# Kernel optimization log

Hardware: AMD Instinct MI355X
Metric: run time of the kernel (lower is better)

Reference implementation:

```python
import jax, jax.numpy as jnp
import numpy as np

NUM_HEADS = 8
NUM_NEIGHBORS = 32


def setup_inputs() -> dict:
    key = jax.random.key(0)
    ks = jax.random.split(key, 5)
    B, S, F, C = 4, 2048, 512, 3
    x = jax.random.normal(ks[0], (B, S, F), dtype=jnp.float32)
    coords = jax.random.uniform(ks[1], (B, S, C), dtype=jnp.float32)
    scale = 1.0 / np.sqrt(F)
    Wq = jax.random.normal(ks[2], (F, F), dtype=jnp.float32) * scale
    Wk = jax.random.normal(ks[3], (F, F), dtype=jnp.float32) * scale
    Wv = jax.random.normal(ks[4], (F, F), dtype=jnp.float32) * scale
    return {"x": x, "coords": coords, "Wq": Wq, "Wk": Wk, "Wv": Wv}


def _nearest_neighbors(coords, k):
    # coords: [B,S,C] -> dists [B,S,S]; drop self (index 0 after argsort)
    diff = coords[:, None, :, :] - coords[:, :, None, :]
    dists = jnp.linalg.norm(diff, axis=-1)
    return jnp.argsort(dists, axis=-1)[:, :, 1:k + 1]  # [B,S,K]


def reference(x, coords, Wq, Wk, Wv):
    B, S, F = x.shape
    H = NUM_HEADS
    D = F // H

    nn_idx = _nearest_neighbors(coords, NUM_NEIGHBORS)  # [B,S,K] int
    # dense boolean neighbor mask [B,S,S]: mask[b,q,kv] = kv in nn_idx[b,q]
    b_ix = jnp.arange(B)[:, None, None]
    q_ix = jnp.arange(S)[None, :, None]
    mask = jnp.zeros((B, S, S), dtype=bool).at[b_ix, q_ix, nn_idx].set(True)

    q = (x @ Wq.T).reshape(B, S, H, D).transpose(0, 2, 1, 3)  # [B,H,S,D]
    k = (x @ Wk.T).reshape(B, S, H, D).transpose(0, 2, 1, 3)
    v = (x @ Wv.T).reshape(B, S, H, D).transpose(0, 2, 1, 3)

    scale = 1.0 / jnp.sqrt(jnp.asarray(D, dtype=x.dtype))
    scores = jnp.einsum("bhqd,bhkd->bhqk", q, k) * scale
    neg_inf = jnp.asarray(-jnp.inf, dtype=scores.dtype)
    scores = jnp.where(mask[:, None, :, :], scores, neg_inf)
    attn = jax.nn.softmax(scores, axis=-1)
    out = jnp.einsum("bhqk,bhkd->bhqd", attn, v)  # [B,H,S,D]
    out = out.transpose(0, 2, 1, 3).reshape(B, S, F)
    metric = k.mean(axis=2)  # [B,H,D]
    return out, metric
```

## Files before the change

kernel.cpp:

```cpp
#include <hip/hip_runtime.h>
#include <stdint.h>

#define BATCH 4
#define SEQ   2048
#define FDIM  512
#define NHEAD 8
#define HDIM  64
#define KNN   32

typedef unsigned int u32;
typedef unsigned long long u64;
typedef unsigned short u16;
typedef unsigned short bf16_t;

typedef __attribute__((ext_vector_type(8))) short short8;
typedef __attribute__((ext_vector_type(4))) float f32x4;

#define SF  ((size_t)SEQ * FDIM)
#define BSF ((size_t)BATCH * SF)

#define CAST_NB 2432
#define XPART_NB 128

__device__ __forceinline__ bf16_t f2bf(float f) {
    u32 x = __float_as_uint(f);
    return (bf16_t)((x + 0x7FFFu + ((x >> 16) & 1u)) >> 16);
}
__device__ __forceinline__ float bf2f(bf16_t u) { return __uint_as_float(((u32)u) << 16); }
__device__ __forceinline__ void bf2x2(u32 p, float& a, float& b) {
    a = __uint_as_float(p << 16);
    b = __uint_as_float(p & 0xFFFF0000u);
}
__device__ __forceinline__ u64 min_u64(u64 a, u64 b) { return a < b ? a : b; }
__device__ __forceinline__ u64 shfl_xor_u64(u64 v, int m) {
    int lo = __shfl_xor((int)(u32)v, m, 64);
    int hi = __shfl_xor((int)(u32)(v >> 32), m, 64);
    return (((u64)(u32)hi) << 32) | (u32)lo;
}

__device__ __forceinline__ void gld16(const bf16_t* gp, bf16_t* lp) {
    __builtin_amdgcn_global_load_lds(
        (const __attribute__((address_space(1))) u32*)gp,
        (__attribute__((address_space(3))) u32*)lp, 16, 0, 0);
}

template <int CTRL>
__device__ __forceinline__ float dppf(float x) {
    return __int_as_float(__builtin_amdgcn_update_dpp(
        0, __float_as_int(x), CTRL, 0xF, 0xF, true));
}

__device__ __forceinline__ float dot8(uint4 k, f32x4 qa, f32x4 qb) {
    float f0, f1, f2, f3, f4, f5, f6, f7;
    bf2x2(k.x, f0, f1); bf2x2(k.y, f2, f3);
    bf2x2(k.z, f4, f5); bf2x2(k.w, f6, f7);
    return qa.x * f0 + qa.y * f1 + qa.z * f2 + qa.w * f3
         + qb.x * f4 + qb.y * f5 + qb.z * f6 + qb.w * f7;
}

__device__ __forceinline__ void acc8(uint4 v, float w, float* o) {
    float f0, f1, f2, f3, f4, f5, f6, f7;
    bf2x2(v.x, f0, f1); bf2x2(v.y, f2, f3);
    bf2x2(v.z, f4, f5); bf2x2(v.w, f6, f7);
    o[0] += w * f0; o[1] += w * f1; o[2] += w * f2; o[3] += w * f3;
    o[4] += w * f4; o[5] += w * f5; o[6] += w * f6; o[7] += w * f7;
}

__device__ __forceinline__ void cast_body(int cid,
                                          const float* __restrict__ x,
                                          const float* __restrict__ wq,
                                          const float* __restrict__ wk,
                                          const float* __restrict__ wv,
                                          bf16_t* __restrict__ xb,
                                          bf16_t* __restrict__ wqb,
                                          bf16_t* __restrict__ wkb,
                                          bf16_t* __restrict__ wvb) {
    int z, blk;
    if (cid < 2048) { z = 0; blk = cid; }
    else { int d = cid - 2048; z = 1 + (d >> 7); blk = d & 127; }
    const float* src = (z == 0) ? x : (z == 1) ? wq : (z == 2) ? wk : wv;
    bf16_t* dst      = (z == 0) ? xb : (z == 1) ? wqb : (z == 2) ? wkb : wvb;
    size_t idx = (size_t)blk * 256 + threadIdx.x;
    const float4 a = ((const float4*)src)[idx * 2 + 0];
    const float4 b = ((const float4*)src)[idx * 2 + 1];
    uint4 o;
    o.x = (u32)f2bf(a.x) | ((u32)f2bf(a.y) << 16);
    o.y = (u32)f2bf(a.z) | ((u32)f2bf(a.w) << 16);
    o.z = (u32)f2bf(b.x) | ((u32)f2bf(b.y) << 16);
    o.w = (u32)f2bf(b.z) | ((u32)f2bf(b.w) << 16);
    ((uint4*)dst)[idx] = o;
}

__device__ __forceinline__ void xpart_body(int id, const float* __restrict__ x,
                                           float* __restrict__ xpart) {
    const int b = id >> 5, chunk = id & 31;
    const int tid = threadIdx.x;
    const float* xp = x + (size_t)b * SF + (size_t)chunk * 64 * FDIM;
    float s0 = 0.f, s1 = 0.f;
    for (int r = 0; r < 64; ++r) {
        s0 += xp[(size_t)r * FDIM + tid];
        s1 += xp[(size_t)r * FDIM + tid + 256];
    }
    float* dst = xpart + (size_t)id * FDIM;
    dst[tid]       = s0 * (1.f / 2048.f);
    dst[tid + 256] = s1 * (1.f / 2048.f);
}

__device__ __forceinline__ void knn_body(char* smem, int blk,
                                         const float* __restrict__ coords,
                                         u16* __restrict__ nn_out) {
    u32* chist = (u32*)smem;
    u32* fhist = (u32*)(smem + 256);
    u64* bk    = (u64*)(smem + 1280);
    u64* wpart = (u64*)(smem + 1792);
    u32* sc    = (u32*)(smem + 1824);
    const int b   = blk >> 11;
    const int qi  = blk & (SEQ - 1);
    const int t   = threadIdx.x;
    const int wid = t >> 6, lane = t & 63;
    const size_t qb = (size_t)blk * KNN;

    fhist[t & 255] = 0;
    if (t < 64) chist[t] = 0;
    if (t == 0) { sc[2] = 0; sc[3] = 0; }

    const float* cb = coords + (size_t)b * SEQ * 3;
    const float qx = cb[qi * 3 + 0];
    const float qy = cb[qi * 3 + 1];
    const float qz = cb[qi * 3 + 2];

    float dist[8];
    int   ib[8];
    u64 tmin = ~0ull;
#pragma unroll
    for (int i = 0; i < 8; ++i) {
        int c = i * 256 + t;
        float dx = __fsub_rn(cb[c * 3 + 0], qx);
        float dy = __fsub_rn(cb[c * 3 + 1], qy);
        float dz = __fsub_rn(cb[c * 3 + 2], qz);
        float d2 = __fadd_rn(__fadd_rn(__fmul_rn(dx, dx), __fmul_rn(dy, dy)),
                             __fmul_rn(dz, dz));
        dist[i] = __fsqrt_rn(d2);
        ib[i] = (int)(dist[i] * 8192.0f);
        u64 key = (((u64)__float_as_uint(dist[i])) << 32) | (u32)c;
        tmin = min_u64(tmin, key);
    }
    tmin = min_u64(tmin, shfl_xor_u64(tmin, 1));
    tmin = min_u64(tmin, shfl_xor_u64(tmin, 2));
    tmin = min_u64(tmin, shfl_xor_u64(tmin, 4));
    tmin = min_u64(tmin, shfl_xor_u64(tmin, 8));
    tmin = min_u64(tmin, shfl_xor_u64(tmin, 16));
    tmin = min_u64(tmin, shfl_xor_u64(tmin, 32));
    if (lane == 0) wpart[wid] = tmin;
    __syncthreads();

#pragma unroll
    for (int i = 0; i < 8; ++i) atomicAdd(&chist[ib[i] >> 8], 1u);
    const u64 M = min_u64(min_u64(wpart[0], wpart[1]),
                          min_u64(wpart[2], wpart[3]));
    __syncthreads();

    if (t < 64) {
        u32 h = chist[t];
        u32 cum = h;
#pragma unroll
        for (int d = 1; d < 64; d <<= 1) {
            u32 v = (u32)__shfl_up((int)cum, d, 64);
            if (t >= d) cum += v;
        }
        u64 bal = __ballot(cum >= 33);
        int Bc = __ffsll((long long)bal) - 1;
        u32 excl = cum - h;
        u32 base = (u32)__shfl((int)excl, Bc, 64);
        if (t == 0) { sc[0] = (u32)Bc; sc[1] = base; }
    }
    __syncthreads();

    {
        const int Bc = (int)sc[0];
#pragma unroll
        for (int i = 0; i < 8; ++i)
            if ((ib[i] >> 8) == Bc) atomicAdd(&fhist[ib[i] & 255], 1u);
    }
    __syncthreads();

    if (t < 64) {
        const u32 Bc = sc[0], base = sc[1];
        u32 f0 = fhist[t * 4 + 0], f1 = fhist[t * 4 + 1];
        u32 f2 = fhist[t * 4 + 2], f3 = fhist[t * 4 + 3];
        u32 s = f0 + f1 + f2 + f3;
        u32 cum = s;
#pragma unroll
        for (int d = 1; d < 64; d <<= 1) {
            u32 v = (u32)__shfl_up((int)cum, d, 64);
            if (t >= d) cum += v;
        }
        u32 E = base + (cum - s);
        u32 c0 = E + f0, c1 = c0 + f1, c2 = c1 + f2, c3 = c2 + f3;
        u64 bal = __ballot(c3 >= 33);
        int L = __ffsll((long long)bal) - 1;
        if (t == L) {
            int j = (c0 >= 33) ? 0 : (c1 >= 33) ? 1 : (c2 >= 33) ? 2 : 3;
            sc[4] = (Bc << 8) | (u32)(t * 4 + j);
        }
    }
    __syncthreads();

    {
        const int ibt = (int)sc[4];
#pragma unroll
        for (int i = 0; i < 8; ++i) {
            int c = i * 256 + t;
            u64 key = (((u64)__float_as_uint(dist[i])) << 32) | (u32)c;
            if (ib[i] < ibt) {
                if (key != M) {
                    u32 pos = atomicAdd(&sc[2], 1u);
                    nn_out[qb + pos] = (u16)c;
                }
            } else if (ib[i] == ibt) {
                u32 bp = atomicAdd(&sc[3], 1u);
                if (bp < 64) bk[bp] = key;
            }
        }
    }
    __syncthreads();

    if (t < 64) {
        const u32 m = sc[2];
        const int n = (int)min(sc[3], 64u);
        const int need = 32 - (int)m;
        u64 k = (t < n) ? bk[t] : ~0ull;
        if (k == M) k = ~0ull;
#pragma unroll 1
        for (int r = 0; r < need; ++r) {
            u64 g = k;
            g = min_u64(g, shfl_xor_u64(g, 1));
            g = min_u64(g, shfl_xor_u64(g, 2));
            g = min_u64(g, shfl_xor_u64(g, 4));
            g = min_u64(g, shfl_xor_u64(g, 8));
            g = min_u64(g, shfl_xor_u64(g, 16));
            g = min_u64(g, shfl_xor_u64(g, 32));
            if (k == g) {
                nn_out[qb + m + r] = (u16)(g & 0x7FF);
                k = ~0ull;
            }
        }
    }
}

__global__ __launch_bounds__(256) void fused_ck(const float* __restrict__ x,
                                                const float* __restrict__ wq,
                                                const float* __restrict__ wk,
                                                const float* __restrict__ wv,
                                                bf16_t* __restrict__ xb,
                                                bf16_t* __restrict__ wqb,
                                                bf16_t* __restrict__ wkb,
                                                bf16_t* __restrict__ wvb,
                                                const float* __restrict__ coords,
                                                u16* __restrict__ nn_out,
                                                float* __restrict__ xpart) {
    __shared__ __align__(16) char smem[1856];
    const int bid = blockIdx.x;
    if (bid < CAST_NB) {
        cast_body(bid, x, wq, wk, wv, xb, wqb, wkb, wvb);
    } else if (bid < CAST_NB + XPART_NB) {
        xpart_body(bid - CAST_NB, x, xpart);
    } else {
        knn_body(smem, bid - CAST_NB - XPART_NB, coords, nn_out);
    }
}

__global__ __launch_bounds__(256) void gemm_mfma(const bf16_t* __restrict__ xb,
                                                 const bf16_t* __restrict__ wqb,
                                                 const bf16_t* __restrict__ wkb,
                                                 const bf16_t* __restrict__ wvb,
                                                 float* __restrict__ qout,
                                                 bf16_t* __restrict__ kvout,
                                                 const float* __restrict__ xpart,
                                                 const float* __restrict__ Wkf,
                                                 float* __restrict__ metric) {
    __shared__ __align__(16) bf16_t As[128 * 32];
    __shared__ __align__(16) bf16_t Bs[128 * 32];
    const int z = blockIdx.z;
    const int tid  = threadIdx.x;

    if (z == 3) {
        const int id = blockIdx.y * 4 + blockIdx.x;
        if (id >= 8) return;
        float* xbarL = (float*)As;
        const int b = id >> 1;
        float a0 = 0.f, a1 = 0.f;
#pragma unroll 4
        for (int c = 0; c < 32; ++c) {
            const float* xp = xpart + (size_t)((b << 5) | c) * FDIM;
            a0 += xp[tid];
            a1 += xp[tid + 256];
        }
        xbarL[tid] = a0; xbarL[tid + 256] = a1;
        __syncthreads();
        const int f = ((id & 1) << 8) | tid;
        const float* wr = Wkf + (size_t)f * FDIM;
        float acc = 0.f;
#pragma unroll 4
        for (int kk = 0; kk < FDIM; kk += 4) {
            float4 wv = *(const float4*)(wr + kk);
            acc += xbarL[kk + 0] * wv.x + xbarL[kk + 1] * wv.y
                 + xbarL[kk + 2] * wv.z + xbarL[kk + 3] * wv.w;
        }
        metric[(b << 9) | f] = acc;
        return;
    }

    const bf16_t* W = (z == 0) ? wqb : (z == 1) ? wkb : wvb;
    const int wid  = tid >> 6, lane = tid & 63;
    const int m16  = lane & 15, quad = lane >> 4;
    const int wm   = (wid & 1) * 64;
    const int wn   = (wid >> 1) * 64;
    const int m0   = blockIdx.y * 128;
    const int n0   = blockIdx.x * 128;

    const int sr = tid >> 2, sc = (tid & 3) * 8;
    const bf16_t* agp = xb + (size_t)(m0 + sr) * FDIM + sc;
    const bf16_t* bgp = W  + (size_t)(n0 + sr) * FDIM + sc;
    bf16_t* lAs = As + tid * 8;
    bf16_t* lBs = Bs + tid * 8;

    f32x4 acc[4][4];
#pragma unroll
    for (int i = 0; i < 4; ++i)
#pragma unroll
        for (int j = 0; j < 4; ++j) acc[i][j] = (f32x4){0.f, 0.f, 0.f, 0.f};

#pragma unroll 1
    for (int k0 = 0; k0 < FDIM; k0 += 32) {
        __syncthreads();
        gld16(agp + k0,                      lAs);
        gld16(agp + (size_t)64 * FDIM + k0,  lAs + 2048);
        gld16(bgp + k0,                      lBs);
        gld16(bgp + (size_t)64 * FDIM + k0,  lBs + 2048);
        __asm__ volatile("s_waitcnt vmcnt(0)" ::: "memory");
        __syncthreads();

        short8 af[4], bfr[4];
#pragma unroll
        for (int i = 0; i < 4; ++i)
            af[i] = *(const short8*)(As + (wm + i * 16 + m16) * 32 + quad * 8);
#pragma unroll
        for (int j = 0; j < 4; ++j)
            bfr[j] = *(const short8*)(Bs + (wn + j * 16 + m16) * 32 + quad * 8);
#pragma unroll
        for (int i = 0; i < 4; ++i)
#pragma unroll
            for (int j = 0; j < 4; ++j)
                acc[i][j] = __builtin_amdgcn_mfma_f32_16x16x32_bf16(af[i], bfr[j],
                                                                    acc[i][j], 0, 0, 0);
    }

    if (z == 0) {
#pragma unroll
        for (int i = 0; i < 4; ++i) {
            const int rowb = m0 + wm + i * 16 + quad * 4;
#pragma unroll
            for (int r = 0; r < 4; ++r) {
                float* orow = qout + (size_t)(rowb + r) * FDIM + n0 + wn + m16;
                orow[ 0] = acc[i][0][r]; orow[16] = acc[i][1][r];
                orow[32] = acc[i][2][r]; orow[48] = acc[i][3][r];
            }
        }
    } else {
        bf16_t* base = kvout + (size_t)(z - 1) * BSF;
#pragma unroll
        for (int i = 0; i < 4; ++i) {
            const int rowb = m0 + wm + i * 16 + quad * 4;
#pragma unroll
            for (int r = 0; r < 4; ++r) {
                bf16_t* orow = base + (size_t)(rowb + r) * FDIM + n0 + wn + m16;
                orow[ 0] = f2bf(acc[i][0][r]); orow[16] = f2bf(acc[i][1][r]);
                orow[32] = f2bf(acc[i][2][r]); orow[48] = f2bf(acc[i][3][r]);
            }
        }
    }
}

__global__ __launch_bounds__(256, 6) void attn_kernel(const bf16_t* __restrict__ kv,
                                                      const u16* __restrict__ nn,
                                                      float* __restrict__ out) {
    __shared__ float qsl[4][64];
    __shared__ float osl[4][8][64];
    const int i   = blockIdx.x;
    const int b   = (i & 7) >> 1;
    const int jb  = ((i >> 3) << 1) | (i & 1);
    const int tid = threadIdx.x;
    const int wid = tid >> 6, lane = tid & 63;
    const int gid = (jb << 2) | wid;
    const int qi  = gid >> 3, h = gid & 7;
    const int blk = (b << 11) | qi;

    int sreg = 0;
    if (lane < KNN) sreg = (int)nn[(size_t)blk * KNN + lane] & (SEQ - 1);
    qsl[wid][lane] = out[(size_t)blk * FDIM + h * HDIM + lane];

    const int g3 = lane >> 3, l8 = lane & 7;
    const int r0 = __shfl(sreg,      g3, 64);
    const int r1 = __shfl(sreg,  8 + g3, 64);
    const int r2 = __shfl(sreg, 16 + g3, 64);
    const int r3 = __shfl(sreg, 24 + g3, 64);

    const bf16_t* base = kv + ((size_t)(b << 11)) * FDIM + h * HDIM + l8 * 8;
    const uint4 k0 = *(const uint4*)(base + (size_t)r0 * FDIM);
    const uint4 k1 = *(const uint4*)(base + (size_t)r1 * FDIM);
    const uint4 k2 = *(const uint4*)(base + (size_t)r2 * FDIM);
    const uint4 k3 = *(const uint4*)(base + (size_t)r3 * FDIM);
    const uint4 v0 = *(const uint4*)(base + BSF + (size_t)r0 * FDIM);
    const uint4 v1 = *(const uint4*)(base + BSF + (size_t)r1 * FDIM);
    const uint4 v2 = *(const uint4*)(base + BSF + (size_t)r2 * FDIM);
    const uint4 v3 = *(const uint4*)(base + BSF + (size_t)r3 * FDIM);

    __asm__ volatile("s_waitcnt lgkmcnt(0)" ::: "memory");
    __builtin_amdgcn_wave_barrier();
    const f32x4 qa = *(const f32x4*)&qsl[wid][l8 * 8];
    const f32x4 qb = *(const f32x4*)&qsl[wid][l8 * 8 + 4];

    float s0 = dot8(k0, qa, qb);
    float s1 = dot8(k1, qa, qb);
    float s2 = dot8(k2, qa, qb);
    float s3 = dot8(k3, qa, qb);
    s0 += dppf<0xB1>(s0); s0 += dppf<0x4E>(s0); s0 += dppf<0x141>(s0);
    s1 += dppf<0xB1>(s1); s1 += dppf<0x4E>(s1); s1 += dppf<0x141>(s1);
    s2 += dppf<0xB1>(s2); s2 += dppf<0x4E>(s2); s2 += dppf<0x141>(s2);
    s3 += dppf<0xB1>(s3); s3 += dppf<0x4E>(s3); s3 += dppf<0x141>(s3);
    s0 *= 0.125f; s1 *= 0.125f; s2 *= 0.125f; s3 *= 0.125f;

    float ml = fmaxf(fmaxf(s0, s1), fmaxf(s2, s3));
    ml = fmaxf(ml, dppf<0x140>(ml));
    ml = fmaxf(ml, __shfl_xor(ml, 16, 64));
    ml = fmaxf(ml, __shfl_xor(ml, 32, 64));
    const float e0 = __expf(s0 - ml), e1 = __expf(s1 - ml);
    const float e2 = __expf(s2 - ml), e3 = __expf(s3 - ml);
    float sl = (e0 + e1) + (e2 + e3);
    sl += dppf<0x140>(sl);
    sl += __shfl_xor(sl, 16, 64);
    sl += __shfl_xor(sl, 32, 64);
    const float rs = 1.0f / sl;
    const float w0 = e0 * rs, w1 = e1 * rs, w2 = e2 * rs, w3 = e3 * rs;

    float o[8] = {0.f, 0.f, 0.f, 0.f, 0.f, 0.f, 0.f, 0.f};
    acc8(v0, w0, o);
    acc8(v1, w1, o);
    acc8(v2, w2, o);
    acc8(v3, w3, o);

    *(f32x4*)&osl[wid][g3][l8 * 8]     = (f32x4){o[0], o[1], o[2], o[3]};
    *(f32x4*)&osl[wid][g3][l8 * 8 + 4] = (f32x4){o[4], o[5], o[6], o[7]};
    __asm__ volatile("s_waitcnt lgkmcnt(0)" ::: "memory");
    __builtin_amdgcn_wave_barrier();
    float r = osl[wid][0][lane];
#pragma unroll
    for (int g = 1; g < 8; ++g) r += osl[wid][g][lane];
    out[(size_t)blk * FDIM + h * HDIM + lane] = r;
}

extern "C" void kernel_launch(void* const* d_in, const int* in_sizes, int n_in,
                              void* d_out, int out_size, void* d_ws, size_t ws_size,
                              hipStream_t stream) {
    const float* x      = (const float*)d_in[0];
    const float* coords = (const float*)d_in[1];
    const float* Wq     = (const float*)d_in[2];
    const float* Wk     = (const float*)d_in[3];
    const float* Wv     = (const float*)d_in[4];
    float* out    = (float*)d_out;
    float* metric = out + BSF;

    char* p = (char*)d_ws;
    bf16_t* xb    = (bf16_t*)p;                      p += BSF * sizeof(bf16_t);
    bf16_t* wqb   = (bf16_t*)p;                      p += (size_t)FDIM * FDIM * sizeof(bf16_t);
    bf16_t* wkb   = (bf16_t*)p;                      p += (size_t)FDIM * FDIM * sizeof(bf16_t);
    bf16_t* wvb   = (bf16_t*)p;                      p += (size_t)FDIM * FDIM * sizeof(bf16_t);
    bf16_t* kv    = (bf16_t*)p;                      p += 2 * BSF * sizeof(bf16_t);
    u16*    nn    = (u16*)p;                         p += (size_t)BATCH * SEQ * KNN * sizeof(u16);
    float*  xpart = (float*)p;

    fused_ck<<<CAST_NB + XPART_NB + BATCH * SEQ, 256, 0, stream>>>(
        x, Wq, Wk, Wv, xb, wqb, wkb, wvb, coords, nn, xpart);

    gemm_mfma<<<dim3(FDIM / 128, (BATCH * SEQ) / 128, 4), 256, 0, stream>>>(
        xb, wqb, wkb, wvb, out, kv, xpart, Wk, metric);

    attn_kernel<<<BATCH * SEQ * NHEAD / 4, 256, 0, stream>>>(kv, nn, out);
}
```

Measured before the change: 163.2 us.

## Run one KNN query per wavefront instead of per block, dropping block barriers

The nearest-neighbour selection now assigns each query to a single 64-lane wavefront, so a 256-thread block handles four queries, each with its own shared-memory slice. Each lane now covers 32 candidates instead of 8. Block-wide __syncthreads and the shared-memory broadcasts of the histogram results are replaced by wave barriers and shuffles, and the KNN block count drops fourfold. The aim is to cut synchronisation overhead and per-block launch cost, in exchange for higher register pressure from the 32-entry distance array and more serial work per lane.

```diff
diff --git a/kernel.cpp b/kernel.cpp
--- a/kernel.cpp
+++ b/kernel.cpp
@@ -21,6 +21,7 @@
 
 #define CAST_NB 2432
 #define XPART_NB 128
+#define KNN_NB  2048
 
 __device__ __forceinline__ bf16_t f2bf(float f) {
     u32 x = __float_as_uint(f);
@@ -106,43 +107,40 @@
     dst[tid + 256] = s1 * (1.f / 2048.f);
 }
 
-__device__ __forceinline__ void knn_body(char* smem, int blk,
+__device__ __forceinline__ void knn_wave(char* wbase, int blk,
                                          const float* __restrict__ coords,
                                          u16* __restrict__ nn_out) {
-    u32* chist = (u32*)smem;
-    u32* fhist = (u32*)(smem + 256);
-    u64* bk    = (u64*)(smem + 1280);
-    u64* wpart = (u64*)(smem + 1792);
-    u32* sc    = (u32*)(smem + 1824);
-    const int b   = blk >> 11;
-    const int qi  = blk & (SEQ - 1);
-    const int t   = threadIdx.x;
-    const int wid = t >> 6, lane = t & 63;
+    u32* chist = (u32*)wbase;
+    u32* fhist = (u32*)(wbase + 256);
+    u64* bk    = (u64*)(wbase + 1280);
+    u32* sc    = (u32*)(wbase + 1792);
+    const int b    = blk >> 11;
+    const int qi   = blk & (SEQ - 1);
+    const int lane = threadIdx.x & 63;
     const size_t qb = (size_t)blk * KNN;
 
-    fhist[t & 255] = 0;
-    if (t < 64) chist[t] = 0;
-    if (t == 0) { sc[2] = 0; sc[3] = 0; }
+    chist[lane] = 0;
+    *(uint4*)&fhist[lane * 4] = (uint4){0u, 0u, 0u, 0u};
+    if (lane == 0) { sc[0] = 0; sc[1] = 0; }
 
     const float* cb = coords + (size_t)b * SEQ * 3;
     const float qx = cb[qi * 3 + 0];
     const float qy = cb[qi * 3 + 1];
     const float qz = cb[qi * 3 + 2];
 
-    float dist[8];
-    int   ib[8];
+    u32 dbits[32];
     u64 tmin = ~0ull;
 #pragma unroll
-    for (int i = 0; i < 8; ++i) {
-        int c = i * 256 + t;
+    for (int i = 0; i < 32; ++i) {
+        int c = i * 64 + lane;
         float dx = __fsub_rn(cb[c * 3 + 0], qx);
         float dy = __fsub_rn(cb[c * 3 + 1], qy);
         float dz = __fsub_rn(cb[c * 3 + 2], qz);
         float d2 = __fadd_rn(__fadd_rn(__fmul_rn(dx, dx), __fmul_rn(dy, dy)),
                              __fmul_rn(dz, dz));
-        dist[i] = __fsqrt_rn(d2);
-        ib[i] = (int)(dist[i] * 8192.0f);
-        u64 key = (((u64)__float_as_uint(dist[i])) << 32) | (u32)c;
+        float dist = __fsqrt_rn(d2);
+        dbits[i] = __float_as_uint(dist);
+        u64 key = (((u64)dbits[i]) << 32) | (u32)c;
         tmin = min_u64(tmin, key);
     }
     tmin = min_u64(tmin, shfl_xor_u64(tmin, 1));
@@ -151,85 +149,84 @@
     tmin = min_u64(tmin, shfl_xor_u64(tmin, 8));
     tmin = min_u64(tmin, shfl_xor_u64(tmin, 16));
     tmin = min_u64(tmin, shfl_xor_u64(tmin, 32));
-    if (lane == 0) wpart[wid] = tmin;
-    __syncthreads();
-
-#pragma unroll
-    for (int i = 0; i < 8; ++i) atomicAdd(&chist[ib[i] >> 8], 1u);
-    const u64 M = min_u64(min_u64(wpart[0], wpart[1]),
-                          min_u64(wpart[2], wpart[3]));
-    __syncthreads();
-
-    if (t < 64) {
-        u32 h = chist[t];
+    const u64 M = tmin;
+
+    __asm__ volatile("s_waitcnt lgkmcnt(0)" ::: "memory");
+    __builtin_amdgcn_wave_barrier();
+
+#pragma unroll
+    for (int i = 0; i < 32; ++i) {
+        int ib = (int)(__uint_as_float(dbits[i]) * 8192.0f);
+        atomicAdd(&chist[ib >> 8], 1u);
+    }
+    __asm__ volatile("s_waitcnt lgkmcnt(0)" ::: "memory");
+    __builtin_amdgcn_wave_barrier();
+
+    int Bc; u32 base;
+    {
+        u32 h = chist[lane];
         u32 cum = h;
 #pragma unroll
         for (int d = 1; d < 64; d <<= 1) {
             u32 v = (u32)__shfl_up((int)cum, d, 64);
-            if (t >= d) cum += v;
+            if (lane >= d) cum += v;
         }
         u64 bal = __ballot(cum >= 33);
-        int Bc = __ffsll((long long)bal) - 1;
-        u32 excl = cum - h;
-        u32 base = (u32)__shfl((int)excl, Bc, 64);
-        if (t == 0) { sc[0] = (u32)Bc; sc[1] = base; }
-    }
-    __syncthreads();
-
+        Bc = __ffsll((long long)bal) - 1;
+        base = (u32)__shfl((int)(cum - h), Bc, 64);
+    }
+
+#pragma unroll
+    for (int i = 0; i < 32; ++i) {
+        int ib = (int)(__uint_as_float(dbits[i]) * 8192.0f);
+        if ((ib >> 8) == Bc) atomicAdd(&fhist[ib & 255], 1u);
+    }
+    __asm__ volatile("s_waitcnt lgkmcnt(0)" ::: "memory");
+    __builtin_amdgcn_wave_barrier();
+
+    int ibt;
     {
-        const int Bc = (int)sc[0];
-#pragma unroll
-        for (int i = 0; i < 8; ++i)
-            if ((ib[i] >> 8) == Bc) atomicAdd(&fhist[ib[i] & 255], 1u);
-    }
-    __syncthreads();
-
-    if (t < 64) {
-        const u32 Bc = sc[0], base = sc[1];
-        u32 f0 = fhist[t * 4 + 0], f1 = fhist[t * 4 + 1];
-        u32 f2 = fhist[t * 4 + 2], f3 = fhist[t * 4 + 3];
+        u32 f0 = fhist[lane * 4 + 0], f1 = fhist[lane * 4 + 1];
+        u32 f2 = fhist[lane * 4 + 2], f3 = fhist[lane * 4 + 3];
         u32 s = f0 + f1 + f2 + f3;
         u32 cum = s;
 #pragma unroll
         for (int d = 1; d < 64; d <<= 1) {
             u32 v = (u32)__shfl_up((int)cum, d, 64);
-            if (t >= d) cum += v;
+            if (lane >= d) cum += v;
         }
         u32 E = base + (cum - s);
         u32 c0 = E + f0, c1 = c0 + f1, c2 = c1 + f2, c3 = c2 + f3;
         u64 bal = __ballot(c3 >= 33);
         int L = __ffsll((long long)bal) - 1;
-        if (t == L) {
-            int j = (c0 >= 33) ? 0 : (c1 >= 33) ? 1 : (c2 >= 33) ? 2 : 3;
-            sc[4] = (Bc << 8) | (u32)(t * 4 + j);
-        }
-    }
-    __syncthreads();
+        int j = (c0 >= 33) ? 0 : (c1 >= 33) ? 1 : (c2 >= 33) ? 2 : 3;
+        int ibt_local = (Bc << 8) | (lane * 4 + j);
+        ibt = __shfl(ibt_local, L, 64);
+    }
+
+#pragma unroll
+    for (int i = 0; i < 32; ++i) {
+        int c = i * 64 + lane;
+        int ib = (int)(__uint_as_float(dbits[i]) * 8192.0f);
+        u64 key = (((u64)dbits[i]) << 32) | (u32)c;
+        if (ib < ibt) {
+            if (key != M) {
+                u32 pos = atomicAdd(&sc[0], 1u);
+                nn_out[qb + pos] = (u16)c;
+            }
+        } else if (ib == ibt) {
+            u32 bp = atomicAdd(&sc[1], 1u);
+            if (bp < 64) bk[bp] = key;
+        }
+    }
+    __asm__ volatile("s_waitcnt lgkmcnt(0)" ::: "memory");
+    __builtin_amdgcn_wave_barrier();
 
     {
-        const int ibt = (int)sc[4];
-#pragma unroll
-        for (int i = 0; i < 8; ++i) {
-            int c = i * 256 + t;
-            u64 key = (((u64)__float_as_uint(dist[i])) << 32) | (u32)c;
-            if (ib[i] < ibt) {
-                if (key != M) {
-                    u32 pos = atomicAdd(&sc[2], 1u);
-                    nn_out[qb + pos] = (u16)c;
-                }
-            } else if (ib[i] == ibt) {
-                u32 bp = atomicAdd(&sc[3], 1u);
-                if (bp < 64) bk[bp] = key;
-            }
-        }
-    }
-    __syncthreads();
-
-    if (t < 64) {
-        const u32 m = sc[2];
-        const int n = (int)min(sc[3], 64u);
+        const u32 m = sc[0];
+        const int n = (int)min(sc[1], 64u);
         const int need = 32 - (int)m;
-        u64 k = (t < n) ? bk[t] : ~0ull;
+        u64 k = (lane < n) ? bk[lane] : ~0ull;
         if (k == M) k = ~0ull;
 #pragma unroll 1
         for (int r = 0; r < need; ++r) {
@@ -259,14 +256,16 @@
                                                 const float* __restrict__ coords,
                                                 u16* __restrict__ nn_out,
                                                 float* __restrict__ xpart) {
-    __shared__ __align__(16) char smem[1856];
+    __shared__ __align__(16) char smem[4 * 1856];
     const int bid = blockIdx.x;
     if (bid < CAST_NB) {
         cast_body(bid, x, wq, wk, wv, xb, wqb, wkb, wvb);
     } else if (bid < CAST_NB + XPART_NB) {
         xpart_body(bid - CAST_NB, x, xpart);
     } else {
-        knn_body(smem, bid - CAST_NB - XPART_NB, coords, nn_out);
+        const int wid = threadIdx.x >> 6;
+        const int blk = (bid - CAST_NB - XPART_NB) * 4 + wid;
+        knn_wave(smem + wid * 1856, blk, coords, nn_out);
     }
 }
 
@@ -480,7 +479,7 @@
     u16*    nn    = (u16*)p;                         p += (size_t)BATCH * SEQ * KNN * sizeof(u16);
     float*  xpart = (float*)p;
 
-    fused_ck<<<CAST_NB + XPART_NB + BATCH * SEQ, 256, 0, stream>>>(
+    fused_ck<<<CAST_NB + XPART_NB + KNN_NB, 256, 0, stream>>>(
         x, Wq, Wk, Wv, xb, wqb, wkb, wvb, coords, nn, xpart);
 
     gemm_mfma<<<dim3(FDIM / 128, (BATCH * SEQ) / 128, 4), 256, 0, stream>>>(
```

Result: slower. 170.2 us (+4.2%).
